# Kernel tuning notes

Measured on AMD Instinct MI355X. Metric: run time of the kernel, lower is better.

Reference implementation:

```python
import jax, jax.numpy as jnp
import numpy as np

NUM_BBOX = 2
NUM_CLASSES = 20
NUM_GRID = 7
THR_CONF = 0.5
THR_NMS = 0.3


def _pairwise_iou(b):
    # b: [N,4] ltrb
    lt = jnp.maximum(b[:, None, :2], b[None, :, :2])
    rb = jnp.minimum(b[:, None, 2:], b[None, :, 2:])
    wh = jnp.clip(rb - lt, 0.0)
    inter = wh[..., 0] * wh[..., 1]
    area = jnp.clip(b[:, 2] - b[:, 0], 0.0) * jnp.clip(b[:, 3] - b[:, 1], 0.0)
    union = area[:, None] + area[None, :] - inter
    return inter / jnp.maximum(union, 1e-9)


def _nms_keep(boxes, scores, labels, valid):
    # Greedy per-class NMS over one image's N candidate boxes.
    N = boxes.shape[0]
    order = jnp.argsort(-scores)
    b, l, v = boxes[order], labels[order], valid[order]
    iou = _pairwise_iou(b)
    sup = (iou > THR_NMS) & (l[:, None] == l[None, :])
    idx = jnp.arange(N)

    def body(i, keep):
        suppressed = jnp.any(keep & sup[:, i] & (idx < i))
        return keep.at[i].set(v[i] & ~suppressed)

    keep_sorted = jax.lax.fori_loop(0, N, body, jnp.zeros(N, dtype=bool))
    # scatter back to original order
    return jnp.zeros(N, dtype=bool).at[order].set(keep_sorted)


def _decode(p):
    # p: [B,G,G, nb*4 + nb + nc]
    B, G = p.shape[0], p.shape[1]
    _is = NUM_BBOX * 4
    conf = jax.nn.sigmoid(p[..., _is:_is + NUM_BBOX])          # [B,G,G,nb]
    cls_logits = p[..., _is + NUM_BBOX:]                        # argmax invariant under sigmoid
    boxes = p[..., :_is].reshape(B, G, G, NUM_BBOX, 4)
    col = jnp.arange(G, dtype=p.dtype)[None, None, :, None]     # broadcasts over axis 2
    row = jnp.arange(G, dtype=p.dtype)[None, :, None, None]     # broadcasts over axis 1
    gx = (jax.nn.sigmoid(boxes[..., 0]) + col) / G
    gy = (jax.nn.sigmoid(boxes[..., 1]) + row) / G
    xy = jnp.stack([gx, gy], axis=-1)                           # [B,G,G,nb,2]
    wh = boxes[..., 2:]                                         # raw wh (not sigmoided, as in source)
    ltrb = jnp.concatenate([xy - wh / 2, xy + wh / 2], axis=-1)  # [B,G,G,nb,4]
    labels = jnp.argmax(cls_logits, axis=-1) + 1                # [B,G,G], 1-based as in source
    labels = jnp.broadcast_to(labels[..., None], conf.shape)
    N = G * G * NUM_BBOX
    return (ltrb.reshape(B, N, 4), conf.reshape(B, N),
            labels.reshape(B, N), (conf > THR_CONF).reshape(B, N))


def setup_inputs() -> dict:
    key = jax.random.key(0)
    p = jax.random.normal(key, (8192, NUM_GRID, NUM_GRID, NUM_BBOX * 5 + NUM_CLASSES), dtype=jnp.float32)
    return {"p_yolo": p}


def reference(p_yolo):
    boxes, scores, labels, valid = _decode(p_yolo)
    keep = jax.vmap(_nms_keep)(boxes, scores, labels, valid)
    # Dense padded equivalent of (ids_batch2, p_boxes_ltrb2, p_labels2, p_scores2):
    # valid final detections are the True entries of `keep` (batch id = row index).
    return boxes, scores, labels, keep
```

## Files before the change

### kernel.cpp

```cpp
#include <hip/hip_runtime.h>
#include <math.h>

#define G      7
#define NCELL  49
#define NBOX   98
#define CH     30
#define RAWF   1470
#define BATCH  8192

#define WAVE_SYNC() asm volatile("s_waitcnt lgkmcnt(0)" ::: "memory")

__device__ __forceinline__ float sigmoidf_(float x) {
    return 1.0f / (1.0f + expf(-x));
}
__device__ __forceinline__ float rdlanef(float x, int i) {
    return __int_as_float(__builtin_amdgcn_readlane(__float_as_int(x), i));
}
__device__ __forceinline__ float div7(float x) {
    const float r7 = 1.0f / 7.0f;
    float q0 = x * r7;
    float e  = fmaf(-7.0f, q0, x);
    return fmaf(e, r7, q0);
}

__device__ __forceinline__ void nms_slow(const float4* sbox, const float2* smeta,
                                         int V, int lane, float4 mb, float2 mm,
                                         float mlab, unsigned long long& k0,
                                         unsigned long long& k1) {
    const double UD = (double)0.3f + 0x1p-26;
    const int i2c = (lane + 64 < NBOX) ? lane + 64 : NBOX - 1;
    const float4 mb2 = sbox[i2c];
    const float2 mm2 = smeta[i2c];
    const float mlab2 = (lane + 64 < V) ? mm2.y : -1.0f;
    for (int i = 0; i < V; ++i) {
        float bx, by, bz, bw, ba, bl;
        if (i < 64) {
            bx = rdlanef(mb.x, i);  by = rdlanef(mb.y, i);
            bz = rdlanef(mb.z, i);  bw = rdlanef(mb.w, i);
            ba = rdlanef(mm.x, i);  bl = rdlanef(mlab, i);
        } else {
            bx = rdlanef(mb2.x, i - 64);  by = rdlanef(mb2.y, i - 64);
            bz = rdlanef(mb2.z, i - 64);  bw = rdlanef(mb2.w, i - 64);
            ba = rdlanef(mm2.x, i - 64);  bl = rdlanef(mlab2, i - 64);
        }
        float w1 = fmaxf(fminf(bz, mb.z) - fmaxf(bx, mb.x), 0.0f);
        float h1 = fmaxf(fminf(bw, mb.w) - fmaxf(by, mb.y), 0.0f);
        float i1 = w1 * h1;
        float u1 = fmaxf(ba + mm.x - i1, 1e-9f);
        bool hit1 = ((double)i1 > UD * (double)u1) && (bl == mlab);
        float w2 = fmaxf(fminf(bz, mb2.z) - fmaxf(bx, mb2.x), 0.0f);
        float h2 = fmaxf(fminf(bw, mb2.w) - fmaxf(by, mb2.y), 0.0f);
        float i2 = w2 * h2;
        float u2 = fmaxf(ba + mm2.x - i2, 1e-9f);
        bool hit2 = ((double)i2 > UD * (double)u2) && (bl == mlab2);
        unsigned long long row0 = __ballot(hit1);
        unsigned long long row1 = __ballot(hit2);
        if (((row0 & k0) | (row1 & k1)) == 0ull) {
            if (i < 64) k0 |= 1ull << i;
            else        k1 |= 1ull << (i - 64);
        }
    }
}

__global__ __launch_bounds__(128, 8) void yolo_nms_kernel(
    const float* __restrict__ p,
    float* __restrict__ out_boxes,
    float* __restrict__ out_scores,
    float* __restrict__ out_labels,
    float* __restrict__ out_keep)
{
#pragma clang fp contract(off)
    __shared__ __align__(16) float4 sboxS[2][NBOX];
    __shared__ __align__(8)  float2 smetaS[2][NBOX];

    const int lane = threadIdx.x & 63;
    const int wv   = threadIdx.x >> 6;
    const int b    = blockIdx.x * 2 + wv;

    float4* sbox  = sboxS[wv];
    float2* smeta = smetaS[wv];

    const float* base = p + (size_t)b * RAWF;

    float4 bb0 = make_float4(0.f, 0.f, 0.f, 0.f);
    float4 bb1 = make_float4(0.f, 0.f, 0.f, 0.f);
    float s0 = -1.0f, s1 = -1.0f, area0 = 0.0f, area1 = 0.0f, lab = 0.0f;
    bool vld0 = false, vld1 = false, act0 = false, act1 = false;

    if (lane < NCELL) {
        const float2* q2 = (const float2*)(base + lane * CH);
        float2 xy0 = q2[0];
        float2 wh0 = q2[1];
        float2 xy1 = q2[2];
        float2 wh1 = q2[3];
        float2 cf  = q2[4];
        float2 c0 = q2[5];
        float bx = c0.x; int ix = 0;
        float by = c0.y; int iy = 1;
        #pragma unroll
        for (int k2 = 1; k2 < 10; ++k2) {
            float2 cv = q2[5 + k2];
            if (cv.x > bx) { bx = cv.x; ix = 2 * k2; }
            if (cv.y > by) { by = cv.y; iy = 2 * k2 + 1; }
        }
        const int bi = (by > bx) ? iy : ix;
        lab = (float)(bi + 1);

        const int r = lane / G, c = lane - r * G;
        float gx0 = div7(sigmoidf_(xy0.x) + (float)c);
        float gy0 = div7(sigmoidf_(xy0.y) + (float)r);
        float gx1 = div7(sigmoidf_(xy1.x) + (float)c);
        float gy1 = div7(sigmoidf_(xy1.y) + (float)r);
        float hx0 = wh0.x * 0.5f, hy0 = wh0.y * 0.5f;
        float hx1 = wh1.x * 0.5f, hy1 = wh1.y * 0.5f;
        bb0 = make_float4(gx0 - hx0, gy0 - hy0, gx0 + hx0, gy0 + hy0);
        bb1 = make_float4(gx1 - hx1, gy1 - hy1, gx1 + hx1, gy1 + hy1);
        area0 = fmaxf(bb0.z - bb0.x, 0.0f) * fmaxf(bb0.w - bb0.y, 0.0f);
        area1 = fmaxf(bb1.z - bb1.x, 0.0f) * fmaxf(bb1.w - bb1.y, 0.0f);
        s0 = sigmoidf_(cf.x);
        s1 = sigmoidf_(cf.y);
        vld0 = (s0 > 0.5f);
        vld1 = (s1 > 0.5f);
        act0 = vld0 && (area0 > 0.0f);
        act1 = vld1 && (area1 > 0.0f);

        float4* ob = (float4*)(out_boxes + (size_t)b * (NBOX * 4));
        ob[2 * lane]     = bb0;
        ob[2 * lane + 1] = bb1;
        ((float2*)(out_scores + (size_t)b * NBOX))[lane] = make_float2(s0, s1);
        ((float2*)(out_labels + (size_t)b * NBOX))[lane] = make_float2(lab, lab);
    }

    unsigned long long m0 = __ballot(act0);
    unsigned long long m1 = __ballot(act1);
    const int V = __popcll(m0) + __popcll(m1);

    int rk0 = 0, rk1 = 0;
    unsigned long long t0 = m0;
    while (t0) {
        int jl = __builtin_ctzll(t0); t0 &= t0 - 1ull;
        float sj = rdlanef(s0, jl);
        rk0 += (sj > s0) || ((sj == s0) && (jl <  lane));
        rk1 += (sj > s1) || ((sj == s1) && (jl <= lane));
    }
    unsigned long long t1 = m1;
    while (t1) {
        int jl = __builtin_ctzll(t1); t1 &= t1 - 1ull;
        float sj = rdlanef(s1, jl);
        rk0 += (sj > s0) || ((sj == s0) && (jl < lane));
        rk1 += (sj > s1) || ((sj == s1) && (jl < lane));
    }

    if (act0) { sbox[rk0] = bb0; smeta[rk0] = make_float2(area0, lab); }
    if (act1) { sbox[rk1] = bb1; smeta[rk1] = make_float2(area1, lab); }
    WAVE_SYNC();
    const float4 mb = sbox[lane];
    const float2 mm = smeta[lane];
    const float mlab = (lane < V) ? mm.y : -1.0f;

    unsigned long long k0 = 0ull, k1 = 0ull;
    const double UD = (double)0.3f + 0x1p-26;

#define ROW_HIT_LDS(BI, MI, HIT) do {                                    \
        float w = fmaxf(fminf((BI).z, mb.z) - fmaxf((BI).x, mb.x), 0.0f);\
        float h = fmaxf(fminf((BI).w, mb.w) - fmaxf((BI).y, mb.y), 0.0f);\
        float inter = w * h;                                             \
        float uc = fmaxf((MI).x + mm.x - inter, 1e-9f);                  \
        HIT = ((double)inter > UD * (double)uc) && ((MI).y == mlab);     \
    } while (0)

    if (V <= 64) {
        int i = 0;
        for (; i + 4 <= V; i += 4) {
            float4 bA = sbox[i],     bB = sbox[i + 1];
            float4 bC = sbox[i + 2], bD = sbox[i + 3];
            float2 mA = smeta[i],     mB = smeta[i + 1];
            float2 mC = smeta[i + 2], mD = smeta[i + 3];
            bool hA, hB, hC, hD;
            ROW_HIT_LDS(bA, mA, hA);
            ROW_HIT_LDS(bB, mB, hB);
            ROW_HIT_LDS(bC, mC, hC);
            ROW_HIT_LDS(bD, mD, hD);
            unsigned long long rA = __ballot(hA);
            unsigned long long rB = __ballot(hB);
            unsigned long long rC = __ballot(hC);
            unsigned long long rD = __ballot(hD);
            k0 |= ((rA & k0) == 0ull) ? (1ull << i) : 0ull;
            k0 |= ((rB & k0) == 0ull) ? (1ull << (i + 1)) : 0ull;
            k0 |= ((rC & k0) == 0ull) ? (1ull << (i + 2)) : 0ull;
            k0 |= ((rD & k0) == 0ull) ? (1ull << (i + 3)) : 0ull;
        }
        for (; i < V; ++i) {
            float4 bA = sbox[i];
            float2 mA = smeta[i];
            bool hA;
            ROW_HIT_LDS(bA, mA, hA);
            unsigned long long rA = __ballot(hA);
            k0 |= ((rA & k0) == 0ull) ? (1ull << i) : 0ull;
        }
    } else {
        nms_slow(sbox, smeta, V, lane, mb, mm, mlab, k0, k1);
    }
#undef ROW_HIT_LDS

    float kv0 = 0.0f, kv1 = 0.0f;
    if (vld0) kv0 = act0 ? (float)((((rk0 < 64) ? k0 : k1) >> (rk0 & 63)) & 1ull) : 1.0f;
    if (vld1) kv1 = act1 ? (float)((((rk1 < 64) ? k0 : k1) >> (rk1 & 63)) & 1ull) : 1.0f;
    if (lane < NCELL)
        ((float2*)(out_keep + (size_t)b * NBOX))[lane] = make_float2(kv0, kv1);
}

extern "C" void kernel_launch(void* const* d_in, const int* in_sizes, int n_in,
                              void* d_out, int out_size, void* d_ws, size_t ws_size,
                              hipStream_t stream) {
    const float* p = (const float*)d_in[0];
    float* out = (float*)d_out;
    float* out_boxes  = out;
    float* out_scores = out + (size_t)BATCH * NBOX * 4;
    float* out_labels = out_scores + (size_t)BATCH * NBOX;
    float* out_keep   = out_labels + (size_t)BATCH * NBOX;

    yolo_nms_kernel<<<BATCH / 2, 128, 0, stream>>>(p, out_boxes, out_scores,
                                                   out_labels, out_keep);
}
```

Before: 92.50 us.

## Process two images per wave with register prefetch of the next image

Each wave now handles two consecutive images instead of one. It loads the raw cell data for the next image into registers while it decodes and runs NMS on the current image, so global load latency overlaps with compute. The grid is halved and the launch bound occupancy hint drops from 8 to 4. The cost is about 30 extra VGPRs for the prefetch buffer and fewer waves in flight to hide latency.

```diff
diff --git a/kernel.cpp b/kernel.cpp
--- a/kernel.cpp
+++ b/kernel.cpp
@@ -7,6 +7,7 @@
 #define CH     30
 #define RAWF   1470
 #define BATCH  8192
+#define NB     2
 
 #define WAVE_SYNC() asm volatile("s_waitcnt lgkmcnt(0)" ::: "memory")
 
@@ -62,7 +63,7 @@
     }
 }
 
-__global__ __launch_bounds__(128, 8) void yolo_nms_kernel(
+__global__ __launch_bounds__(128, 4) void yolo_nms_kernel(
     const float* __restrict__ p,
     float* __restrict__ out_boxes,
     float* __restrict__ out_scores,
@@ -75,91 +76,106 @@
 
     const int lane = threadIdx.x & 63;
     const int wv   = threadIdx.x >> 6;
-    const int b    = blockIdx.x * 2 + wv;
+    const int wave = blockIdx.x * 2 + wv;
+    const int b0   = wave * NB;
 
     float4* sbox  = sboxS[wv];
     float2* smeta = smetaS[wv];
 
-    const float* base = p + (size_t)b * RAWF;
-
-    float4 bb0 = make_float4(0.f, 0.f, 0.f, 0.f);
-    float4 bb1 = make_float4(0.f, 0.f, 0.f, 0.f);
-    float s0 = -1.0f, s1 = -1.0f, area0 = 0.0f, area1 = 0.0f, lab = 0.0f;
-    bool vld0 = false, vld1 = false, act0 = false, act1 = false;
-
+    float2 cur[15], nxt[15];
     if (lane < NCELL) {
-        const float2* q2 = (const float2*)(base + lane * CH);
-        float2 xy0 = q2[0];
-        float2 wh0 = q2[1];
-        float2 xy1 = q2[2];
-        float2 wh1 = q2[3];
-        float2 cf  = q2[4];
-        float2 c0 = q2[5];
-        float bx = c0.x; int ix = 0;
-        float by = c0.y; int iy = 1;
+        const float2* q2 = (const float2*)(p + (size_t)b0 * RAWF + lane * CH);
         #pragma unroll
-        for (int k2 = 1; k2 < 10; ++k2) {
-            float2 cv = q2[5 + k2];
-            if (cv.x > bx) { bx = cv.x; ix = 2 * k2; }
-            if (cv.y > by) { by = cv.y; iy = 2 * k2 + 1; }
-        }
-        const int bi = (by > bx) ? iy : ix;
-        lab = (float)(bi + 1);
-
-        const int r = lane / G, c = lane - r * G;
-        float gx0 = div7(sigmoidf_(xy0.x) + (float)c);
-        float gy0 = div7(sigmoidf_(xy0.y) + (float)r);
-        float gx1 = div7(sigmoidf_(xy1.x) + (float)c);
-        float gy1 = div7(sigmoidf_(xy1.y) + (float)r);
-        float hx0 = wh0.x * 0.5f, hy0 = wh0.y * 0.5f;
-        float hx1 = wh1.x * 0.5f, hy1 = wh1.y * 0.5f;
-        bb0 = make_float4(gx0 - hx0, gy0 - hy0, gx0 + hx0, gy0 + hy0);
-        bb1 = make_float4(gx1 - hx1, gy1 - hy1, gx1 + hx1, gy1 + hy1);
-        area0 = fmaxf(bb0.z - bb0.x, 0.0f) * fmaxf(bb0.w - bb0.y, 0.0f);
-        area1 = fmaxf(bb1.z - bb1.x, 0.0f) * fmaxf(bb1.w - bb1.y, 0.0f);
-        s0 = sigmoidf_(cf.x);
-        s1 = sigmoidf_(cf.y);
-        vld0 = (s0 > 0.5f);
-        vld1 = (s1 > 0.5f);
-        act0 = vld0 && (area0 > 0.0f);
-        act1 = vld1 && (area1 > 0.0f);
-
-        float4* ob = (float4*)(out_boxes + (size_t)b * (NBOX * 4));
-        ob[2 * lane]     = bb0;
-        ob[2 * lane + 1] = bb1;
-        ((float2*)(out_scores + (size_t)b * NBOX))[lane] = make_float2(s0, s1);
-        ((float2*)(out_labels + (size_t)b * NBOX))[lane] = make_float2(lab, lab);
+        for (int k = 0; k < 15; ++k) cur[k] = q2[k];
     }
 
-    unsigned long long m0 = __ballot(act0);
-    unsigned long long m1 = __ballot(act1);
-    const int V = __popcll(m0) + __popcll(m1);
-
-    int rk0 = 0, rk1 = 0;
-    unsigned long long t0 = m0;
-    while (t0) {
-        int jl = __builtin_ctzll(t0); t0 &= t0 - 1ull;
-        float sj = rdlanef(s0, jl);
-        rk0 += (sj > s0) || ((sj == s0) && (jl <  lane));
-        rk1 += (sj > s1) || ((sj == s1) && (jl <= lane));
-    }
-    unsigned long long t1 = m1;
-    while (t1) {
-        int jl = __builtin_ctzll(t1); t1 &= t1 - 1ull;
-        float sj = rdlanef(s1, jl);
-        rk0 += (sj > s0) || ((sj == s0) && (jl < lane));
-        rk1 += (sj > s1) || ((sj == s1) && (jl < lane));
-    }
-
-    if (act0) { sbox[rk0] = bb0; smeta[rk0] = make_float2(area0, lab); }
-    if (act1) { sbox[rk1] = bb1; smeta[rk1] = make_float2(area1, lab); }
-    WAVE_SYNC();
-    const float4 mb = sbox[lane];
-    const float2 mm = smeta[lane];
-    const float mlab = (lane < V) ? mm.y : -1.0f;
-
-    unsigned long long k0 = 0ull, k1 = 0ull;
-    const double UD = (double)0.3f + 0x1p-26;
+    #pragma unroll
+    for (int it = 0; it < NB; ++it) {
+        const int b = b0 + it;
+
+        if (it + 1 < NB && lane < NCELL) {
+            const float2* qn = (const float2*)(p + (size_t)(b + 1) * RAWF + lane * CH);
+            #pragma unroll
+            for (int k = 0; k < 15; ++k) nxt[k] = qn[k];
+        }
+
+        float4 bb0 = make_float4(0.f, 0.f, 0.f, 0.f);
+        float4 bb1 = make_float4(0.f, 0.f, 0.f, 0.f);
+        float s0 = -1.0f, s1 = -1.0f, area0 = 0.0f, area1 = 0.0f, lab = 0.0f;
+        bool vld0 = false, vld1 = false, act0 = false, act1 = false;
+
+        if (lane < NCELL) {
+            float2 xy0 = cur[0];
+            float2 wh0 = cur[1];
+            float2 xy1 = cur[2];
+            float2 wh1 = cur[3];
+            float2 cf  = cur[4];
+            float2 c0 = cur[5];
+            float bx = c0.x; int ix = 0;
+            float by = c0.y; int iy = 1;
+            #pragma unroll
+            for (int k2 = 1; k2 < 10; ++k2) {
+                float2 cv = cur[5 + k2];
+                if (cv.x > bx) { bx = cv.x; ix = 2 * k2; }
+                if (cv.y > by) { by = cv.y; iy = 2 * k2 + 1; }
+            }
+            const int bi = (by > bx) ? iy : ix;
+            lab = (float)(bi + 1);
+
+            const int r = lane / G, c = lane - r * G;
+            float gx0 = div7(sigmoidf_(xy0.x) + (float)c);
+            float gy0 = div7(sigmoidf_(xy0.y) + (float)r);
+            float gx1 = div7(sigmoidf_(xy1.x) + (float)c);
+            float gy1 = div7(sigmoidf_(xy1.y) + (float)r);
+            float hx0 = wh0.x * 0.5f, hy0 = wh0.y * 0.5f;
+            float hx1 = wh1.x * 0.5f, hy1 = wh1.y * 0.5f;
+            bb0 = make_float4(gx0 - hx0, gy0 - hy0, gx0 + hx0, gy0 + hy0);
+            bb1 = make_float4(gx1 - hx1, gy1 - hy1, gx1 + hx1, gy1 + hy1);
+            area0 = fmaxf(bb0.z - bb0.x, 0.0f) * fmaxf(bb0.w - bb0.y, 0.0f);
+            area1 = fmaxf(bb1.z - bb1.x, 0.0f) * fmaxf(bb1.w - bb1.y, 0.0f);
+            s0 = sigmoidf_(cf.x);
+            s1 = sigmoidf_(cf.y);
+            vld0 = (s0 > 0.5f);
+            vld1 = (s1 > 0.5f);
+            act0 = vld0 && (area0 > 0.0f);
+            act1 = vld1 && (area1 > 0.0f);
+
+            float4* ob = (float4*)(out_boxes + (size_t)b * (NBOX * 4));
+            ob[2 * lane]     = bb0;
+            ob[2 * lane + 1] = bb1;
+            ((float2*)(out_scores + (size_t)b * NBOX))[lane] = make_float2(s0, s1);
+            ((float2*)(out_labels + (size_t)b * NBOX))[lane] = make_float2(lab, lab);
+        }
+
+        unsigned long long m0 = __ballot(act0);
+        unsigned long long m1 = __ballot(act1);
+        const int V = __popcll(m0) + __popcll(m1);
+
+        int rk0 = 0, rk1 = 0;
+        unsigned long long t0 = m0;
+        while (t0) {
+            int jl = __builtin_ctzll(t0); t0 &= t0 - 1ull;
+            float sj = rdlanef(s0, jl);
+            rk0 += (sj > s0) || ((sj == s0) && (jl <  lane));
+            rk1 += (sj > s1) || ((sj == s1) && (jl <= lane));
+        }
+        unsigned long long t1 = m1;
+        while (t1) {
+            int jl = __builtin_ctzll(t1); t1 &= t1 - 1ull;
+            float sj = rdlanef(s1, jl);
+            rk0 += (sj > s0) || ((sj == s0) && (jl < lane));
+            rk1 += (sj > s1) || ((sj == s1) && (jl < lane));
+        }
+
+        if (act0) { sbox[rk0] = bb0; smeta[rk0] = make_float2(area0, lab); }
+        if (act1) { sbox[rk1] = bb1; smeta[rk1] = make_float2(area1, lab); }
+        WAVE_SYNC();
+        const float4 mb = sbox[lane];
+        const float2 mm = smeta[lane];
+        const float mlab = (lane < V) ? mm.y : -1.0f;
+
+        unsigned long long k0 = 0ull, k1 = 0ull;
+        const double UD = (double)0.3f + 0x1p-26;
 
 #define ROW_HIT_LDS(BI, MI, HIT) do {                                    \
         float w = fmaxf(fminf((BI).z, mb.z) - fmaxf((BI).x, mb.x), 0.0f);\
@@ -169,45 +185,51 @@
         HIT = ((double)inter > UD * (double)uc) && ((MI).y == mlab);     \
     } while (0)
 
-    if (V <= 64) {
-        int i = 0;
-        for (; i + 4 <= V; i += 4) {
-            float4 bA = sbox[i],     bB = sbox[i + 1];
-            float4 bC = sbox[i + 2], bD = sbox[i + 3];
-            float2 mA = smeta[i],     mB = smeta[i + 1];
-            float2 mC = smeta[i + 2], mD = smeta[i + 3];
-            bool hA, hB, hC, hD;
-            ROW_HIT_LDS(bA, mA, hA);
-            ROW_HIT_LDS(bB, mB, hB);
-            ROW_HIT_LDS(bC, mC, hC);
-            ROW_HIT_LDS(bD, mD, hD);
-            unsigned long long rA = __ballot(hA);
-            unsigned long long rB = __ballot(hB);
-            unsigned long long rC = __ballot(hC);
-            unsigned long long rD = __ballot(hD);
-            k0 |= ((rA & k0) == 0ull) ? (1ull << i) : 0ull;
-            k0 |= ((rB & k0) == 0ull) ? (1ull << (i + 1)) : 0ull;
-            k0 |= ((rC & k0) == 0ull) ? (1ull << (i + 2)) : 0ull;
-            k0 |= ((rD & k0) == 0ull) ? (1ull << (i + 3)) : 0ull;
-        }
-        for (; i < V; ++i) {
-            float4 bA = sbox[i];
-            float2 mA = smeta[i];
-            bool hA;
-            ROW_HIT_LDS(bA, mA, hA);
-            unsigned long long rA = __ballot(hA);
-            k0 |= ((rA & k0) == 0ull) ? (1ull << i) : 0ull;
-        }
-    } else {
-        nms_slow(sbox, smeta, V, lane, mb, mm, mlab, k0, k1);
+        if (V <= 64) {
+            int i = 0;
+            for (; i + 4 <= V; i += 4) {
+                float4 bA = sbox[i],     bB = sbox[i + 1];
+                float4 bC = sbox[i + 2], bD = sbox[i + 3];
+                float2 mA = smeta[i],     mB = smeta[i + 1];
+                float2 mC = smeta[i + 2], mD = smeta[i + 3];
+                bool hA, hB, hC, hD;
+                ROW_HIT_LDS(bA, mA, hA);
+                ROW_HIT_LDS(bB, mB, hB);
+                ROW_HIT_LDS(bC, mC, hC);
+                ROW_HIT_LDS(bD, mD, hD);
+                unsigned long long rA = __ballot(hA);
+                unsigned long long rB = __ballot(hB);
+                unsigned long long rC = __ballot(hC);
+                unsigned long long rD = __ballot(hD);
+                k0 |= ((rA & k0) == 0ull) ? (1ull << i) : 0ull;
+                k0 |= ((rB & k0) == 0ull) ? (1ull << (i + 1)) : 0ull;
+                k0 |= ((rC & k0) == 0ull) ? (1ull << (i + 2)) : 0ull;
+                k0 |= ((rD & k0) == 0ull) ? (1ull << (i + 3)) : 0ull;
+            }
+            for (; i < V; ++i) {
+                float4 bA = sbox[i];
+                float2 mA = smeta[i];
+                bool hA;
+                ROW_HIT_LDS(bA, mA, hA);
+                unsigned long long rA = __ballot(hA);
+                k0 |= ((rA & k0) == 0ull) ? (1ull << i) : 0ull;
+            }
+        } else {
+            nms_slow(sbox, smeta, V, lane, mb, mm, mlab, k0, k1);
+        }
+#undef ROW_HIT_LDS
+
+        float kv0 = 0.0f, kv1 = 0.0f;
+        if (vld0) kv0 = act0 ? (float)((((rk0 < 64) ? k0 : k1) >> (rk0 & 63)) & 1ull) : 1.0f;
+        if (vld1) kv1 = act1 ? (float)((((rk1 < 64) ? k0 : k1) >> (rk1 & 63)) & 1ull) : 1.0f;
+        if (lane < NCELL)
+            ((float2*)(out_keep + (size_t)b * NBOX))[lane] = make_float2(kv0, kv1);
+
+        if (it + 1 < NB) {
+            #pragma unroll
+            for (int k = 0; k < 15; ++k) cur[k] = nxt[k];
+        }
     }
-#undef ROW_HIT_LDS
-
-    float kv0 = 0.0f, kv1 = 0.0f;
-    if (vld0) kv0 = act0 ? (float)((((rk0 < 64) ? k0 : k1) >> (rk0 & 63)) & 1ull) : 1.0f;
-    if (vld1) kv1 = act1 ? (float)((((rk1 < 64) ? k0 : k1) >> (rk1 & 63)) & 1ull) : 1.0f;
-    if (lane < NCELL)
-        ((float2*)(out_keep + (size_t)b * NBOX))[lane] = make_float2(kv0, kv1);
 }
 
 extern "C" void kernel_launch(void* const* d_in, const int* in_sizes, int n_in,
@@ -220,6 +242,6 @@
     float* out_labels = out_scores + (size_t)BATCH * NBOX;
     float* out_keep   = out_labels + (size_t)BATCH * NBOX;
 
-    yolo_nms_kernel<<<BATCH / 2, 128, 0, stream>>>(p, out_boxes, out_scores,
-                                                   out_labels, out_keep);
-}
+    yolo_nms_kernel<<<BATCH / (2 * NB), 128, 0, stream>>>(p, out_boxes, out_scores,
+                                                          out_labels, out_keep);
+}
```

Result: slower. 95.66 us (+3.4%).
